# Performance work log

Hardware: AMD Instinct MI355X
Metric: run time of the kernel (lower is better)

Reference implementation:

```python
import jax, jax.numpy as jnp
import numpy as np

N = 50000
E = 800000
F = 128
H = 128
D = 3

def setup_inputs() -> dict:
    key = jax.random.key(0)
    ks = jax.random.split(key, 12)
    s = lambda fan_in: 1.0 / np.sqrt(fan_in)
    return {
        "node": jax.random.normal(ks[0], (N, F), jnp.float32),
        "coordinate": jax.random.normal(ks[1], (N, D), jnp.float32),
        "edge_index": jax.random.randint(ks[2], (2, E), 0, N, jnp.int32),
        "We1": jax.random.normal(ks[3], (2 * F + 1, H), jnp.float32) * s(2 * F + 1),
        "be1": jnp.zeros((H,), jnp.float32),
        "We2": jax.random.normal(ks[4], (H, H), jnp.float32) * s(H),
        "be2": jnp.zeros((H,), jnp.float32),
        "Wx": jax.random.normal(ks[5], (H, 1), jnp.float32) * s(H),
        "bx": jnp.zeros((1,), jnp.float32),
        "Wh1": jax.random.normal(ks[6], (F + H, H), jnp.float32) * s(F + H),
        "bh1": jnp.zeros((H,), jnp.float32),
        "Wh2": jax.random.normal(ks[7], (H, F), jnp.float32) * s(H),
        "bh2": jnp.zeros((F,), jnp.float32),
    }

def reference(node, coordinate, edge_index, We1, be1, We2, be2, Wx, bx, Wh1, bh1, Wh2, bh2):
    src = edge_index[0]
    dst = edge_index[1]
    n = node.shape[0]
    # gather endpoint features / coords
    h_j = node[src]            # [E, F]
    h_i = node[dst]            # [E, F]
    dist = coordinate[dst] - coordinate[src]          # [E, D] = x_i - x_j
    sqdist = jnp.sum(dist * dist, axis=1, keepdims=True)  # [E, 1]
    # phi_e: Linear -> ReLU -> Linear
    e_in = jnp.concatenate([h_i, h_j, sqdist], axis=-1)    # [E, 2F+1]
    m_ij = jax.nn.relu(e_in @ We1 + be1) @ We2 + be2       # [E, H]
    # phi_x: Linear to scalar edge weight
    w_ij = m_ij @ Wx + bx                                  # [E, 1]
    vec = dist * w_ij                                      # [E, D]
    C = 1.0 / (n - 1)
    delta_x = jax.ops.segment_sum(vec, dst, num_segments=n) * C
    x_new = coordinate + delta_x
    # aggregate messages per target node (sum)
    m_i = jax.ops.segment_sum(m_ij, dst, num_segments=n)   # [N, H]
    # phi_h: Linear -> ReLU -> Linear
    h_in = jnp.concatenate([node, m_i], axis=1)            # [N, F+H]
    h_new = jax.nn.relu(h_in @ Wh1 + bh1) @ Wh2 + bh2      # [N, F]
    return (h_new, x_new)
```

## Files before the change

### kernel.cpp

```cpp
#include <hip/hip_runtime.h>
#include <stdint.h>

#define NN 50000
#define NE 800000
#define NBINS 50001
#define H_OUT_OFF 6400000

typedef float  f32x4  __attribute__((ext_vector_type(4)));
typedef short  bf16x8 __attribute__((ext_vector_type(8)));

static __device__ __forceinline__ unsigned short f2b(float f) {
  unsigned u = __float_as_uint(f);
  return (unsigned short)((u + 0x7fffu + ((u >> 16) & 1u)) >> 16);
}
static __device__ __forceinline__ float b2f(unsigned short h) {
  return __uint_as_float(((unsigned)h) << 16);
}

__global__ void k1_kernel(const int* __restrict__ ei,
                          int* __restrict__ cnt,
                          unsigned short* __restrict__ rank,
                          const float* __restrict__ We1,
                          const float* __restrict__ We2,
                          const float* __restrict__ Wh1,
                          const float* __restrict__ Wh2,
                          const float* __restrict__ be2,
                          const float* __restrict__ Wx,
                          const float* __restrict__ bx,
                          unsigned short* __restrict__ We1Ttop,
                          unsigned short* __restrict__ We1Tbot,
                          unsigned short* __restrict__ We2T,
                          unsigned short* __restrict__ Wh1T,
                          unsigned short* __restrict__ Wh2T,
                          float* __restrict__ uvec) {
  int b = blockIdx.x, tid = threadIdx.x;
  if (b < 3125) {
    int i = b * 256 + tid;
    if (i < NE) rank[i] = (unsigned short)atomicAdd(&cnt[ei[NE + i]], 1);
    return;
  }
  b -= 3125;
  if (b < 384) {
    int i = b * 256 + tid;
    if (i < 16384) {
      int n = i >> 7, k = i & 127;
      We1Ttop[i] = f2b(We1[k * 128 + n]);
    } else if (i < 32768) {
      int j = i - 16384; int n = j >> 7, k = j & 127;
      We1Tbot[j] = f2b(We1[(128 + k) * 128 + n]);
    } else if (i < 49152) {
      int j = i - 32768; int n = j >> 7, k = j & 127;
      We2T[j] = f2b(We2[k * 128 + n]);
    } else if (i < 81920) {
      int j = i - 49152; int n = j >> 8, k = j & 255;
      Wh1T[j] = f2b(Wh1[k * 128 + n]);
    } else if (i < 98304) {
      int j = i - 81920; int n = j >> 7, k = j & 127;
      Wh2T[j] = f2b(Wh2[k * 128 + n]);
    }
    return;
  }
  int k = tid;
  if (k < 128) {
    float s = 0.f;
    for (int n = 0; n < 128; n++) s += We2[k * 128 + n] * Wx[n];
    uvec[k] = s;
  } else if (k == 128) {
    float s = 0.f;
    for (int n = 0; n < 128; n++) s += be2[n] * Wx[n];
    uvec[128] = s + bx[0];
  }
}

__global__ void scanA_kernel(const int* __restrict__ cnt, int* __restrict__ bsum) {
  __shared__ int sd[256];
  int b = blockIdx.x, t = threadIdx.x, i = b * 256 + t;
  sd[t] = (i < NBINS) ? cnt[i] : 0;
  __syncthreads();
  for (int s = 128; s; s >>= 1) {
    if (t < s) sd[t] += sd[t + s];
    __syncthreads();
  }
  if (t == 0) bsum[b] = sd[0];
}

__global__ void scanC_kernel(const int* __restrict__ cnt, const int* __restrict__ bsum,
                             int* __restrict__ starts) {
  __shared__ int sd[256];
  int b = blockIdx.x, t = threadIdx.x, i = b * 256 + t;
  int bv = (t < 196) ? bsum[t] : 0;
  sd[t] = bv;
  __syncthreads();
  for (int off = 1; off < 256; off <<= 1) {
    int x = (t >= off) ? sd[t - off] : 0;
    __syncthreads();
    sd[t] += x;
    __syncthreads();
  }
  int boff = (b > 0) ? sd[b - 1] : 0;
  __syncthreads();
  int v = (i < NBINS) ? cnt[i] : 0;
  sd[t] = v;
  __syncthreads();
  for (int off = 1; off < 256; off <<= 1) {
    int x = (t >= off) ? sd[t - off] : 0;
    __syncthreads();
    sd[t] += x;
    __syncthreads();
  }
  if (i < NBINS) starts[i] = sd[t] - v + boff;
}

__global__ __launch_bounds__(256, 4)
void k3_kernel(const int* __restrict__ ei,
               const unsigned short* __restrict__ rank,
               const int* __restrict__ starts,
               unsigned short* __restrict__ srcs,
               const float* __restrict__ node,
               const unsigned short* __restrict__ We1Ttop,
               const unsigned short* __restrict__ We1Tbot,
               const float* __restrict__ be1,
               unsigned short* __restrict__ Yb,
               unsigned short* __restrict__ Zb) {
  __shared__ __align__(16) unsigned short sA[64][136];
  const int tid = threadIdx.x;
  int b = blockIdx.x;

  if (b < 3125) {
    int i = b * 256 + tid;
    if (i < NE) {
      srcs[starts[ei[NE + i]] + (int)rank[i]] = (unsigned short)ei[i];
    }
    return;
  }
  b -= 3125;
  const int n0 = b * 64;

  for (int c = tid; c < 64 * 16; c += 256) {
    int e = c >> 4, s = c & 15;
    int n = n0 + e;
    if (n < NN) {
      const float* p = node + (size_t)n * 128 + s * 8;
      float4 v0 = *(const float4*)p;
      float4 v1 = *(const float4*)(p + 4);
      *(ushort4*)&sA[e][s * 8]     = make_ushort4(f2b(v0.x), f2b(v0.y), f2b(v0.z), f2b(v0.w));
      *(ushort4*)&sA[e][s * 8 + 4] = make_ushort4(f2b(v1.x), f2b(v1.y), f2b(v1.z), f2b(v1.w));
    } else {
      *(uint4*)&sA[e][s * 8] = make_uint4(0, 0, 0, 0);
    }
  }
  __syncthreads();

  const int wave = tid >> 6, lane = tid & 63;
  const int quad = lane >> 4, l16 = lane & 15;
  const int col0 = wave * 32 + l16, col1 = wave * 32 + 16 + l16;

  const f32x4 zero = {0.f, 0.f, 0.f, 0.f};
  f32x4 accY[4][2], accZ[4][2];
#pragma unroll
  for (int mt = 0; mt < 4; mt++) {
    accY[mt][0] = zero; accY[mt][1] = zero;
    accZ[mt][0] = zero; accZ[mt][1] = zero;
  }

#pragma unroll
  for (int kt = 0; kt < 4; kt++) {
    int kb = kt * 32 + quad * 8;
    bf16x8 by0 = *(const bf16x8*)(We1Ttop + (col0 << 7) + kb);
    bf16x8 by1 = *(const bf16x8*)(We1Ttop + (col1 << 7) + kb);
    bf16x8 bz0 = *(const bf16x8*)(We1Tbot + (col0 << 7) + kb);
    bf16x8 bz1 = *(const bf16x8*)(We1Tbot + (col1 << 7) + kb);
#pragma unroll
    for (int mt = 0; mt < 4; mt++) {
      bf16x8 a = *(const bf16x8*)&sA[mt * 16 + l16][kb];
      accY[mt][0] = __builtin_amdgcn_mfma_f32_16x16x32_bf16(a, by0, accY[mt][0], 0, 0, 0);
      accY[mt][1] = __builtin_amdgcn_mfma_f32_16x16x32_bf16(a, by1, accY[mt][1], 0, 0, 0);
      accZ[mt][0] = __builtin_amdgcn_mfma_f32_16x16x32_bf16(a, bz0, accZ[mt][0], 0, 0, 0);
      accZ[mt][1] = __builtin_amdgcn_mfma_f32_16x16x32_bf16(a, bz1, accZ[mt][1], 0, 0, 0);
    }
  }

  float sb0 = be1[col0], sb1 = be1[col1];
#pragma unroll
  for (int mt = 0; mt < 4; mt++) {
#pragma unroll
    for (int r = 0; r < 4; r++) {
      int row = mt * 16 + quad * 4 + r;
      int n = n0 + row;
      if (n < NN) {
        Yb[(size_t)n * 128 + col0] = f2b(accY[mt][0][r] + sb0);
        Yb[(size_t)n * 128 + col1] = f2b(accY[mt][1][r] + sb1);
        Zb[(size_t)n * 128 + col0] = f2b(accZ[mt][0][r]);
        Zb[(size_t)n * 128 + col1] = f2b(accZ[mt][1][r]);
      }
    }
  }
}

__global__ __launch_bounds__(256, 8)
void edge_kernel(const unsigned short* __restrict__ Zb,
                 const unsigned short* __restrict__ Yb,
                 const unsigned short* __restrict__ srcs,
                 const int* __restrict__ starts,
                 const float* __restrict__ coord,
                 const float* __restrict__ We1,
                 const float* __restrict__ uvec,
                 float* __restrict__ T,
                 float* __restrict__ out) {
  __shared__ int    sSrc[4][64];
  __shared__ float4 sQ[4][64];

  const int tid = threadIdx.x, wave = tid >> 6, lane = tid & 63;
  const int n = blockIdx.x * 4 + wave;
  const int half = lane >> 5, l32 = lane & 31;
  const int col = l32 * 4;

  const int start = starts[n], end = starts[n + 1];

  const float4 wsq = *(const float4*)(We1 + 256 * 128 + col);
  const float4 u   = *(const float4*)(uvec + col);
  const float  c   = uvec[128];
  ushort4 yv = *(const ushort4*)(Yb + (size_t)n * 128 + col);
  const float y0 = b2f(yv.x), y1 = b2f(yv.y), y2 = b2f(yv.z), y3 = b2f(yv.w);
  const float cdx = coord[n * 3 + 0], cdy = coord[n * 3 + 1], cdz = coord[n * 3 + 2];

  float aT0 = 0.f, aT1 = 0.f, aT2 = 0.f, aT3 = 0.f;
  float sx = 0.f, sy = 0.f, sz = 0.f;
  float dsx = 0.f, dsy = 0.f, dsz = 0.f;

  for (int cb = start; cb < end; cb += 64) {
    int m = end - cb; if (m > 64) m = 64;
    int s = 0; float dx = 0.f, dy = 0.f, dz = 0.f;
    if (lane < m) {
      s = (int)srcs[cb + lane];
      dx = cdx - coord[s * 3 + 0];
      dy = cdy - coord[s * 3 + 1];
      dz = cdz - coord[s * 3 + 2];
      dsx += dx; dsy += dy; dsz += dz;
    }
    sSrc[wave][lane] = s;
    sQ[wave][lane] = make_float4(dx, dy, dz, dx * dx + dy * dy + dz * dz);
    __builtin_amdgcn_wave_barrier();
    int pairs = (m + 1) >> 1;
    for (int p = 0; p < pairs; p++) {
      int idx = 2 * p + half;
      int ss = sSrc[wave][idx];
      float4 q = sQ[wave][idx];
      float valid = (idx < m) ? 1.f : 0.f;
      ushort4 zv = *(const ushort4*)(Zb + (size_t)ss * 128 + col);
      float t0 = fmaxf(b2f(zv.x) + y0 + q.w * wsq.x, 0.f) * valid;
      float t1 = fmaxf(b2f(zv.y) + y1 + q.w * wsq.y, 0.f) * valid;
      float t2 = fmaxf(b2f(zv.z) + y2 + q.w * wsq.z, 0.f) * valid;
      float t3 = fmaxf(b2f(zv.w) + y3 + q.w * wsq.w, 0.f) * valid;
      aT0 += t0; aT1 += t1; aT2 += t2; aT3 += t3;
      float tu = t0 * u.x + t1 * u.y + t2 * u.z + t3 * u.w;
      sx += tu * q.x; sy += tu * q.y; sz += tu * q.z;
    }
    __builtin_amdgcn_wave_barrier();
  }

  aT0 += __shfl_xor(aT0, 32); aT1 += __shfl_xor(aT1, 32);
  aT2 += __shfl_xor(aT2, 32); aT3 += __shfl_xor(aT3, 32);
  if (half == 0) {
    *(float4*)&T[(size_t)n * 128 + col] = make_float4(aT0, aT1, aT2, aT3);
  }

  float px = sx + c * dsx, py = sy + c * dsy, pz = sz + c * dsz;
#pragma unroll
  for (int o = 1; o < 64; o <<= 1) {
    px += __shfl_xor(px, o); py += __shfl_xor(py, o); pz += __shfl_xor(pz, o);
  }
  if (lane == 0) {
    const float C = 1.0f / 49999.0f;
    out[H_OUT_OFF + n * 3 + 0] = cdx + C * px;
    out[H_OUT_OFF + n * 3 + 1] = cdy + C * py;
    out[H_OUT_OFF + n * 3 + 2] = cdz + C * pz;
  }
}

__global__ __launch_bounds__(256, 3)
void node_kernel(const float* __restrict__ node,
                 const float* __restrict__ T,
                 const int* __restrict__ starts,
                 const unsigned short* __restrict__ We2T,
                 const float* __restrict__ be2,
                 const unsigned short* __restrict__ Wh1T,
                 const float* __restrict__ bh1,
                 const unsigned short* __restrict__ Wh2T,
                 const float* __restrict__ bh2,
                 float* __restrict__ out) {
  __shared__ __align__(16) unsigned short sA[64][264];
  __shared__ __align__(16) unsigned short sT[64][136];
  __shared__ float sDeg[64];

  const int tid = threadIdx.x;
  const int n0 = blockIdx.x * 64;

  if (tid < 64) {
    int n = n0 + tid;
    sDeg[tid] = (n < NN) ? (float)(starts[n + 1] - starts[n]) : 0.f;
  }

  for (int c = tid; c < 64 * 16; c += 256) {
    int e = c >> 4, s = c & 15;
    int n = n0 + e;
    if (n < NN) {
      const float* pn = node + (size_t)n * 128 + s * 8;
      float4 a0 = *(const float4*)pn;
      float4 a1 = *(const float4*)(pn + 4);
      *(ushort4*)&sA[e][s * 8]     = make_ushort4(f2b(a0.x), f2b(a0.y), f2b(a0.z), f2b(a0.w));
      *(ushort4*)&sA[e][s * 8 + 4] = make_ushort4(f2b(a1.x), f2b(a1.y), f2b(a1.z), f2b(a1.w));
      const float* p = T + (size_t)n * 128 + s * 8;
      float4 v0 = *(const float4*)p;
      float4 v1 = *(const float4*)(p + 4);
      *(ushort4*)&sT[e][s * 8]     = make_ushort4(f2b(v0.x), f2b(v0.y), f2b(v0.z), f2b(v0.w));
      *(ushort4*)&sT[e][s * 8 + 4] = make_ushort4(f2b(v1.x), f2b(v1.y), f2b(v1.z), f2b(v1.w));
    } else {
      *(uint4*)&sA[e][s * 8] = make_uint4(0, 0, 0, 0);
      *(uint4*)&sT[e][s * 8] = make_uint4(0, 0, 0, 0);
    }
  }
  __syncthreads();

  const int wave = tid >> 6, lane = tid & 63;
  const int quad = lane >> 4, l16 = lane & 15;
  const int col0 = wave * 32 + l16, col1 = wave * 32 + 16 + l16;

  const f32x4 zero = {0.f, 0.f, 0.f, 0.f};

  f32x4 accM[4][2];
#pragma unroll
  for (int mt = 0; mt < 4; mt++) { accM[mt][0] = zero; accM[mt][1] = zero; }
#pragma unroll
  for (int kt = 0; kt < 4; kt++) {
    int kb = kt * 32 + quad * 8;
    bf16x8 b0 = *(const bf16x8*)(We2T + (col0 << 7) + kb);
    bf16x8 b1 = *(const bf16x8*)(We2T + (col1 << 7) + kb);
#pragma unroll
    for (int mt = 0; mt < 4; mt++) {
      bf16x8 a = *(const bf16x8*)&sT[mt * 16 + l16][kb];
      accM[mt][0] = __builtin_amdgcn_mfma_f32_16x16x32_bf16(a, b0, accM[mt][0], 0, 0, 0);
      accM[mt][1] = __builtin_amdgcn_mfma_f32_16x16x32_bf16(a, b1, accM[mt][1], 0, 0, 0);
    }
  }
  {
    float eb0 = be2[col0], eb1 = be2[col1];
#pragma unroll
    for (int mt = 0; mt < 4; mt++) {
#pragma unroll
      for (int r = 0; r < 4; r++) {
        int row = mt * 16 + quad * 4 + r;
        float dg = sDeg[row];
        sA[row][128 + col0] = f2b(accM[mt][0][r] + dg * eb0);
        sA[row][128 + col1] = f2b(accM[mt][1][r] + dg * eb1);
      }
    }
  }
  __syncthreads();

  f32x4 acc[4][2];
#pragma unroll
  for (int mt = 0; mt < 4; mt++) { acc[mt][0] = zero; acc[mt][1] = zero; }
#pragma unroll
  for (int kt = 0; kt < 8; kt++) {
    int kb = kt * 32 + quad * 8;
    bf16x8 b0 = *(const bf16x8*)(Wh1T + (col0 << 8) + kb);
    bf16x8 b1 = *(const bf16x8*)(Wh1T + (col1 << 8) + kb);
#pragma unroll
    for (int mt = 0; mt < 4; mt++) {
      bf16x8 a = *(const bf16x8*)&sA[mt * 16 + l16][kb];
      acc[mt][0] = __builtin_amdgcn_mfma_f32_16x16x32_bf16(a, b0, acc[mt][0], 0, 0, 0);
      acc[mt][1] = __builtin_amdgcn_mfma_f32_16x16x32_bf16(a, b1, acc[mt][1], 0, 0, 0);
    }
  }
  {
    float sb0 = bh1[col0], sb1 = bh1[col1];
#pragma unroll
    for (int mt = 0; mt < 4; mt++) {
#pragma unroll
      for (int r = 0; r < 4; r++) {
        int row = mt * 16 + quad * 4 + r;
        sT[row][col0] = f2b(fmaxf(acc[mt][0][r] + sb0, 0.f));
        sT[row][col1] = f2b(fmaxf(acc[mt][1][r] + sb1, 0.f));
      }
    }
  }
  __syncthreads();

  f32x4 acc2[4][2];
#pragma unroll
  for (int mt = 0; mt < 4; mt++) { acc2[mt][0] = zero; acc2[mt][1] = zero; }
#pragma unroll
  for (int kt = 0; kt < 4; kt++) {
    int kb = kt * 32 + quad * 8;
    bf16x8 b0 = *(const bf16x8*)(Wh2T + (col0 << 7) + kb);
    bf16x8 b1 = *(const bf16x8*)(Wh2T + (col1 << 7) + kb);
#pragma unroll
    for (int mt = 0; mt < 4; mt++) {
      bf16x8 a = *(const bf16x8*)&sT[mt * 16 + l16][kb];
      acc2[mt][0] = __builtin_amdgcn_mfma_f32_16x16x32_bf16(a, b0, acc2[mt][0], 0, 0, 0);
      acc2[mt][1] = __builtin_amdgcn_mfma_f32_16x16x32_bf16(a, b1, acc2[mt][1], 0, 0, 0);
    }
  }
  {
    float eb0 = bh2[col0], eb1 = bh2[col1];
#pragma unroll
    for (int mt = 0; mt < 4; mt++) {
#pragma unroll
      for (int r = 0; r < 4; r++) {
        int row = mt * 16 + quad * 4 + r;
        int n = n0 + row;
        if (n < NN) {
          out[(size_t)n * 128 + col0] = acc2[mt][0][r] + eb0;
          out[(size_t)n * 128 + col1] = acc2[mt][1][r] + eb1;
        }
      }
    }
  }
}

extern "C" void kernel_launch(void* const* d_in, const int* in_sizes, int n_in,
                              void* d_out, int out_size, void* d_ws, size_t ws_size,
                              hipStream_t stream) {
  const float* node  = (const float*)d_in[0];
  const float* coord = (const float*)d_in[1];
  const int*   ei    = (const int*)d_in[2];
  const float* We1   = (const float*)d_in[3];
  const float* be1   = (const float*)d_in[4];
  const float* We2   = (const float*)d_in[5];
  const float* be2   = (const float*)d_in[6];
  const float* Wx    = (const float*)d_in[7];
  const float* bx    = (const float*)d_in[8];
  const float* Wh1   = (const float*)d_in[9];
  const float* bh1   = (const float*)d_in[10];
  const float* Wh2   = (const float*)d_in[11];
  const float* bh2   = (const float*)d_in[12];
  float* out = (float*)d_out;

  char* ws = (char*)d_ws;
  float*          T      = (float*)(ws);
  int*            cnt    = (int*)  (ws + 25600000);
  int*            starts = (int*)  (ws + 25800704);
  int*            bsum   = (int*)  (ws + 26001408);
  unsigned short* rank   = (unsigned short*)(ws + 26002432);
  unsigned short* srcs   = (unsigned short*)(ws + 27602432);
  unsigned short* Yb     = (unsigned short*)(ws + 29202432);
  unsigned short* Zb     = (unsigned short*)(ws + 42002432);
  unsigned short* We1Ttop= (unsigned short*)(ws + 54802432);
  unsigned short* We1Tbot= (unsigned short*)(ws + 54835200);
  unsigned short* We2T   = (unsigned short*)(ws + 54867968);
  unsigned short* Wh1T   = (unsigned short*)(ws + 54900736);
  unsigned short* Wh2T   = (unsigned short*)(ws + 54966272);
  float*          uvec   = (float*)(ws + 54999040);

  hipMemsetAsync(cnt, 0, 200704, stream);

  k1_kernel<<<3510, 256, 0, stream>>>(ei, cnt, rank, We1, We2, Wh1, Wh2,
                                      be2, Wx, bx,
                                      We1Ttop, We1Tbot, We2T, Wh1T, Wh2T, uvec);
  scanA_kernel<<<196, 256, 0, stream>>>(cnt, bsum);
  scanC_kernel<<<196, 256, 0, stream>>>(cnt, bsum, starts);
  k3_kernel<<<3907, 256, 0, stream>>>(ei, rank, starts, srcs,
                                      node, We1Ttop, We1Tbot, be1, Yb, Zb);
  edge_kernel<<<NN / 4, 256, 0, stream>>>(Zb, Yb, srcs, starts, coord, We1, uvec,
                                          T, out);
  node_kernel<<<782, 256, 0, stream>>>(node, T, starts, We2T, be2,
                                       Wh1T, bh1, Wh2T, bh2, out);
}
```

Measured before the change: 242.0 us.

## Fuse all stages into one persistent cooperative kernel with grid syncs

Replaces the memset and six separate kernel launches with a single cooperative persistent kernel. Phases are separated by grid.sync(), and blocks loop over work with grid-stride loops. This targets launch overhead and inter-kernel gaps. The costs are grid-wide barrier overhead, a grid limited to at most 1024 blocks (so less parallelism in the edge phase), and an occupancy cap from launch_bounds(256,4). The old multi-kernel path stays as a fallback if the cooperative launch fails.

```diff
diff --git a/kernel.cpp b/kernel.cpp
--- a/kernel.cpp
+++ b/kernel.cpp
@@ -1,10 +1,14 @@
 #include <hip/hip_runtime.h>
+#include <hip/hip_cooperative_groups.h>
 #include <stdint.h>
+
+namespace cg = cooperative_groups;
 
 #define NN 50000
 #define NE 800000
 #define NBINS 50001
 #define H_OUT_OFF 6400000
+#define NTILE 782
 
 typedef float  f32x4  __attribute__((ext_vector_type(4)));
 typedef short  bf16x8 __attribute__((ext_vector_type(8)));
@@ -17,15 +21,398 @@
   return __uint_as_float(((unsigned)h) << 16);
 }
 
-__global__ void k1_kernel(const int* __restrict__ ei,
-                          int* __restrict__ cnt,
+__global__ __launch_bounds__(256, 4)
+void mega_kernel(const int* __restrict__ ei,
+                 int* __restrict__ cnt,
+                 unsigned short* __restrict__ rank,
+                 int* __restrict__ starts,
+                 int* __restrict__ bsum,
+                 unsigned short* __restrict__ srcs,
+                 const float* __restrict__ node,
+                 const float* __restrict__ coord,
+                 const float* __restrict__ We1,
+                 const float* __restrict__ be1,
+                 const float* __restrict__ We2,
+                 const float* __restrict__ be2,
+                 const float* __restrict__ Wx,
+                 const float* __restrict__ bx,
+                 const float* __restrict__ Wh1,
+                 const float* __restrict__ bh1,
+                 const float* __restrict__ Wh2,
+                 const float* __restrict__ bh2,
+                 unsigned short* __restrict__ We1Ttop,
+                 unsigned short* __restrict__ We1Tbot,
+                 unsigned short* __restrict__ We2T,
+                 unsigned short* __restrict__ Wh1T,
+                 unsigned short* __restrict__ Wh2T,
+                 float* __restrict__ uvec,
+                 float* __restrict__ T,
+                 unsigned short* __restrict__ Yb,
+                 unsigned short* __restrict__ Zb,
+                 float* __restrict__ out) {
+  __shared__ __align__(16) unsigned char smem[34048];
+  cg::grid_group grid = cg::this_grid();
+  const int tid = threadIdx.x;
+  const int bid = blockIdx.x;
+  const int gridN = gridDim.x;
+  const int wave = tid >> 6, lane = tid & 63;
+
+  for (int i = bid * 256 + tid; i < NBINS; i += gridN * 256) cnt[i] = 0;
+  grid.sync();
+
+  for (int i = bid * 256 + tid; i < NE; i += gridN * 256) {
+    rank[i] = (unsigned short)atomicAdd(&cnt[ei[NE + i]], 1);
+  }
+  for (int i = bid * 256 + tid; i < 98304; i += gridN * 256) {
+    if (i < 16384) {
+      int n = i >> 7, k = i & 127;
+      We1Ttop[i] = f2b(We1[k * 128 + n]);
+    } else if (i < 32768) {
+      int j = i - 16384; int n = j >> 7, k = j & 127;
+      We1Tbot[j] = f2b(We1[(128 + k) * 128 + n]);
+    } else if (i < 49152) {
+      int j = i - 32768; int n = j >> 7, k = j & 127;
+      We2T[j] = f2b(We2[k * 128 + n]);
+    } else if (i < 81920) {
+      int j = i - 49152; int n = j >> 8, k = j & 255;
+      Wh1T[j] = f2b(Wh1[k * 128 + n]);
+    } else {
+      int j = i - 81920; int n = j >> 7, k = j & 127;
+      Wh2T[j] = f2b(Wh2[k * 128 + n]);
+    }
+  }
+  if (bid == 0) {
+    int k = tid;
+    if (k < 128) {
+      float s = 0.f;
+      for (int n = 0; n < 128; n++) s += We2[k * 128 + n] * Wx[n];
+      uvec[k] = s;
+    } else if (k == 128) {
+      float s = 0.f;
+      for (int n = 0; n < 128; n++) s += be2[n] * Wx[n];
+      uvec[128] = s + bx[0];
+    }
+  }
+  grid.sync();
+
+  {
+    int* sd = (int*)smem;
+    for (int ch = bid; ch < 196; ch += gridN) {
+      int i = ch * 256 + tid;
+      sd[tid] = (i < NBINS) ? cnt[i] : 0;
+      __syncthreads();
+      for (int s = 128; s; s >>= 1) {
+        if (tid < s) sd[tid] += sd[tid + s];
+        __syncthreads();
+      }
+      if (tid == 0) bsum[ch] = sd[0];
+      __syncthreads();
+    }
+  }
+  grid.sync();
+
+  {
+    int* sd   = (int*)smem;
+    int* sPre = (int*)smem + 256;
+    int bv = (tid < 196) ? bsum[tid] : 0;
+    sPre[tid] = bv;
+    __syncthreads();
+    for (int off = 1; off < 256; off <<= 1) {
+      int x = (tid >= off) ? sPre[tid - off] : 0;
+      __syncthreads();
+      sPre[tid] += x;
+      __syncthreads();
+    }
+    for (int ch = bid; ch < 196; ch += gridN) {
+      int i = ch * 256 + tid;
+      int boff = (ch > 0) ? sPre[ch - 1] : 0;
+      int v = (i < NBINS) ? cnt[i] : 0;
+      sd[tid] = v;
+      __syncthreads();
+      for (int off = 1; off < 256; off <<= 1) {
+        int x = (tid >= off) ? sd[tid - off] : 0;
+        __syncthreads();
+        sd[tid] += x;
+        __syncthreads();
+      }
+      if (i < NBINS) starts[i] = sd[tid] - v + boff;
+      __syncthreads();
+    }
+  }
+  grid.sync();
+
+  {
+    unsigned short (*sA)[136] = (unsigned short (*)[136])smem;
+    const int quad = lane >> 4, l16 = lane & 15;
+    const int col0 = wave * 32 + l16, col1 = wave * 32 + 16 + l16;
+    const f32x4 zero = {0.f, 0.f, 0.f, 0.f};
+    for (int tb = bid; tb < NTILE; tb += gridN) {
+      const int n0 = tb * 64;
+      for (int c = tid; c < 64 * 16; c += 256) {
+        int e = c >> 4, s = c & 15;
+        int n = n0 + e;
+        if (n < NN) {
+          const float* p = node + (size_t)n * 128 + s * 8;
+          float4 v0 = *(const float4*)p;
+          float4 v1 = *(const float4*)(p + 4);
+          *(ushort4*)&sA[e][s * 8]     = make_ushort4(f2b(v0.x), f2b(v0.y), f2b(v0.z), f2b(v0.w));
+          *(ushort4*)&sA[e][s * 8 + 4] = make_ushort4(f2b(v1.x), f2b(v1.y), f2b(v1.z), f2b(v1.w));
+        } else {
+          *(uint4*)&sA[e][s * 8] = make_uint4(0, 0, 0, 0);
+        }
+      }
+      __syncthreads();
+      f32x4 accY[4][2], accZ[4][2];
+#pragma unroll
+      for (int mt = 0; mt < 4; mt++) {
+        accY[mt][0] = zero; accY[mt][1] = zero;
+        accZ[mt][0] = zero; accZ[mt][1] = zero;
+      }
+#pragma unroll
+      for (int kt = 0; kt < 4; kt++) {
+        int kb = kt * 32 + quad * 8;
+        bf16x8 by0 = *(const bf16x8*)(We1Ttop + (col0 << 7) + kb);
+        bf16x8 by1 = *(const bf16x8*)(We1Ttop + (col1 << 7) + kb);
+        bf16x8 bz0 = *(const bf16x8*)(We1Tbot + (col0 << 7) + kb);
+        bf16x8 bz1 = *(const bf16x8*)(We1Tbot + (col1 << 7) + kb);
+#pragma unroll
+        for (int mt = 0; mt < 4; mt++) {
+          bf16x8 a = *(const bf16x8*)&sA[mt * 16 + l16][kb];
+          accY[mt][0] = __builtin_amdgcn_mfma_f32_16x16x32_bf16(a, by0, accY[mt][0], 0, 0, 0);
+          accY[mt][1] = __builtin_amdgcn_mfma_f32_16x16x32_bf16(a, by1, accY[mt][1], 0, 0, 0);
+          accZ[mt][0] = __builtin_amdgcn_mfma_f32_16x16x32_bf16(a, bz0, accZ[mt][0], 0, 0, 0);
+          accZ[mt][1] = __builtin_amdgcn_mfma_f32_16x16x32_bf16(a, bz1, accZ[mt][1], 0, 0, 0);
+        }
+      }
+      float sb0 = be1[col0], sb1 = be1[col1];
+#pragma unroll
+      for (int mt = 0; mt < 4; mt++) {
+#pragma unroll
+        for (int r = 0; r < 4; r++) {
+          int row = mt * 16 + quad * 4 + r;
+          int n = n0 + row;
+          if (n < NN) {
+            Yb[(size_t)n * 128 + col0] = f2b(accY[mt][0][r] + sb0);
+            Yb[(size_t)n * 128 + col1] = f2b(accY[mt][1][r] + sb1);
+            Zb[(size_t)n * 128 + col0] = f2b(accZ[mt][0][r]);
+            Zb[(size_t)n * 128 + col1] = f2b(accZ[mt][1][r]);
+          }
+        }
+      }
+      __syncthreads();
+    }
+  }
+  for (int i = bid * 256 + tid; i < NE; i += gridN * 256) {
+    srcs[starts[ei[NE + i]] + (int)rank[i]] = (unsigned short)ei[i];
+  }
+  grid.sync();
+
+  {
+    int*    sSrc = (int*)smem + wave * 64;
+    float4* sQ   = (float4*)(smem + 1024) + wave * 64;
+    const int half = lane >> 5, l32 = lane & 31;
+    const int col = l32 * 4;
+    const float4 wsq = *(const float4*)(We1 + 256 * 128 + col);
+    const float4 u   = *(const float4*)(uvec + col);
+    const float  c   = uvec[128];
+
+    for (int vb = bid; vb < NN / 4; vb += gridN) {
+      const int n = vb * 4 + wave;
+      const int start = starts[n], end = starts[n + 1];
+      ushort4 yv = *(const ushort4*)(Yb + (size_t)n * 128 + col);
+      const float y0 = b2f(yv.x), y1 = b2f(yv.y), y2 = b2f(yv.z), y3 = b2f(yv.w);
+      const float cdx = coord[n * 3 + 0], cdy = coord[n * 3 + 1], cdz = coord[n * 3 + 2];
+
+      float aT0 = 0.f, aT1 = 0.f, aT2 = 0.f, aT3 = 0.f;
+      float sx = 0.f, sy = 0.f, sz = 0.f;
+      float dsx = 0.f, dsy = 0.f, dsz = 0.f;
+
+      for (int cb = start; cb < end; cb += 64) {
+        int m = end - cb; if (m > 64) m = 64;
+        int s = 0; float dx = 0.f, dy = 0.f, dz = 0.f;
+        if (lane < m) {
+          s = (int)srcs[cb + lane];
+          dx = cdx - coord[s * 3 + 0];
+          dy = cdy - coord[s * 3 + 1];
+          dz = cdz - coord[s * 3 + 2];
+          dsx += dx; dsy += dy; dsz += dz;
+        }
+        sSrc[lane] = s;
+        sQ[lane] = make_float4(dx, dy, dz, dx * dx + dy * dy + dz * dz);
+        __builtin_amdgcn_wave_barrier();
+        int pairs = (m + 1) >> 1;
+        for (int p = 0; p < pairs; p++) {
+          int idx = 2 * p + half;
+          int ss = sSrc[idx];
+          float4 q = sQ[idx];
+          float valid = (idx < m) ? 1.f : 0.f;
+          ushort4 zv = *(const ushort4*)(Zb + (size_t)ss * 128 + col);
+          float t0 = fmaxf(b2f(zv.x) + y0 + q.w * wsq.x, 0.f) * valid;
+          float t1 = fmaxf(b2f(zv.y) + y1 + q.w * wsq.y, 0.f) * valid;
+          float t2 = fmaxf(b2f(zv.z) + y2 + q.w * wsq.z, 0.f) * valid;
+          float t3 = fmaxf(b2f(zv.w) + y3 + q.w * wsq.w, 0.f) * valid;
+          aT0 += t0; aT1 += t1; aT2 += t2; aT3 += t3;
+          float tu = t0 * u.x + t1 * u.y + t2 * u.z + t3 * u.w;
+          sx += tu * q.x; sy += tu * q.y; sz += tu * q.z;
+        }
+        __builtin_amdgcn_wave_barrier();
+      }
+
+      aT0 += __shfl_xor(aT0, 32); aT1 += __shfl_xor(aT1, 32);
+      aT2 += __shfl_xor(aT2, 32); aT3 += __shfl_xor(aT3, 32);
+      if (half == 0) {
+        *(float4*)&T[(size_t)n * 128 + col] = make_float4(aT0, aT1, aT2, aT3);
+      }
+      float px = sx + c * dsx, py = sy + c * dsy, pz = sz + c * dsz;
+#pragma unroll
+      for (int o = 1; o < 64; o <<= 1) {
+        px += __shfl_xor(px, o); py += __shfl_xor(py, o); pz += __shfl_xor(pz, o);
+      }
+      if (lane == 0) {
+        const float C = 1.0f / 49999.0f;
+        out[H_OUT_OFF + n * 3 + 0] = cdx + C * px;
+        out[H_OUT_OFF + n * 3 + 1] = cdy + C * py;
+        out[H_OUT_OFF + n * 3 + 2] = cdz + C * pz;
+      }
+    }
+  }
+  grid.sync();
+
+  {
+    unsigned short (*sA)[264] = (unsigned short (*)[264])smem;
+    float* sDeg = (float*)(smem + 33792);
+    const int quad = lane >> 4, l16 = lane & 15;
+    const int col0 = wave * 32 + l16, col1 = wave * 32 + 16 + l16;
+    const f32x4 zero = {0.f, 0.f, 0.f, 0.f};
+
+    for (int tb = bid; tb < NTILE; tb += gridN) {
+      const int n0 = tb * 64;
+      if (tid < 64) {
+        int n = n0 + tid;
+        sDeg[tid] = (n < NN) ? (float)(starts[n + 1] - starts[n]) : 0.f;
+      }
+      for (int c = tid; c < 64 * 16; c += 256) {
+        int e = c >> 4, s = c & 15;
+        int n = n0 + e;
+        if (n < NN) {
+          const float* pn = node + (size_t)n * 128 + s * 8;
+          float4 a0 = *(const float4*)pn;
+          float4 a1 = *(const float4*)(pn + 4);
+          *(ushort4*)&sA[e][s * 8]     = make_ushort4(f2b(a0.x), f2b(a0.y), f2b(a0.z), f2b(a0.w));
+          *(ushort4*)&sA[e][s * 8 + 4] = make_ushort4(f2b(a1.x), f2b(a1.y), f2b(a1.z), f2b(a1.w));
+          const float* p = T + (size_t)n * 128 + s * 8;
+          float4 v0 = *(const float4*)p;
+          float4 v1 = *(const float4*)(p + 4);
+          *(ushort4*)&sA[e][128 + s * 8]     = make_ushort4(f2b(v0.x), f2b(v0.y), f2b(v0.z), f2b(v0.w));
+          *(ushort4*)&sA[e][128 + s * 8 + 4] = make_ushort4(f2b(v1.x), f2b(v1.y), f2b(v1.z), f2b(v1.w));
+        } else {
+          *(uint4*)&sA[e][s * 8] = make_uint4(0, 0, 0, 0);
+          *(uint4*)&sA[e][128 + s * 8] = make_uint4(0, 0, 0, 0);
+        }
+      }
+      __syncthreads();
+
+      f32x4 accM[4][2];
+#pragma unroll
+      for (int mt = 0; mt < 4; mt++) { accM[mt][0] = zero; accM[mt][1] = zero; }
+#pragma unroll
+      for (int kt = 0; kt < 4; kt++) {
+        int kb = kt * 32 + quad * 8;
+        bf16x8 b0 = *(const bf16x8*)(We2T + (col0 << 7) + kb);
+        bf16x8 b1 = *(const bf16x8*)(We2T + (col1 << 7) + kb);
+#pragma unroll
+        for (int mt = 0; mt < 4; mt++) {
+          bf16x8 a = *(const bf16x8*)&sA[mt * 16 + l16][128 + kb];
+          accM[mt][0] = __builtin_amdgcn_mfma_f32_16x16x32_bf16(a, b0, accM[mt][0], 0, 0, 0);
+          accM[mt][1] = __builtin_amdgcn_mfma_f32_16x16x32_bf16(a, b1, accM[mt][1], 0, 0, 0);
+        }
+      }
+      __syncthreads();
+      {
+        float eb0 = be2[col0], eb1 = be2[col1];
+#pragma unroll
+        for (int mt = 0; mt < 4; mt++) {
+#pragma unroll
+          for (int r = 0; r < 4; r++) {
+            int row = mt * 16 + quad * 4 + r;
+            float dg = sDeg[row];
+            sA[row][128 + col0] = f2b(accM[mt][0][r] + dg * eb0);
+            sA[row][128 + col1] = f2b(accM[mt][1][r] + dg * eb1);
+          }
+        }
+      }
+      __syncthreads();
+
+      f32x4 acc[4][2];
+#pragma unroll
+      for (int mt = 0; mt < 4; mt++) { acc[mt][0] = zero; acc[mt][1] = zero; }
+#pragma unroll
+      for (int kt = 0; kt < 8; kt++) {
+        int kb = kt * 32 + quad * 8;
+        bf16x8 b0 = *(const bf16x8*)(Wh1T + (col0 << 8) + kb);
+        bf16x8 b1 = *(const bf16x8*)(Wh1T + (col1 << 8) + kb);
+#pragma unroll
+        for (int mt = 0; mt < 4; mt++) {
+          bf16x8 a = *(const bf16x8*)&sA[mt * 16 + l16][kb];
+          acc[mt][0] = __builtin_amdgcn_mfma_f32_16x16x32_bf16(a, b0, acc[mt][0], 0, 0, 0);
+          acc[mt][1] = __builtin_amdgcn_mfma_f32_16x16x32_bf16(a, b1, acc[mt][1], 0, 0, 0);
+        }
+      }
+      __syncthreads();
+      {
+        float sb0 = bh1[col0], sb1 = bh1[col1];
+#pragma unroll
+        for (int mt = 0; mt < 4; mt++) {
+#pragma unroll
+          for (int r = 0; r < 4; r++) {
+            int row = mt * 16 + quad * 4 + r;
+            sA[row][col0] = f2b(fmaxf(acc[mt][0][r] + sb0, 0.f));
+            sA[row][col1] = f2b(fmaxf(acc[mt][1][r] + sb1, 0.f));
+          }
+        }
+      }
+      __syncthreads();
+
+      f32x4 acc2[4][2];
+#pragma unroll
+      for (int mt = 0; mt < 4; mt++) { acc2[mt][0] = zero; acc2[mt][1] = zero; }
+#pragma unroll
+      for (int kt = 0; kt < 4; kt++) {
+        int kb = kt * 32 + quad * 8;
+        bf16x8 b0 = *(const bf16x8*)(Wh2T + (col0 << 7) + kb);
+        bf16x8 b1 = *(const bf16x8*)(Wh2T + (col1 << 7) + kb);
+#pragma unroll
+        for (int mt = 0; mt < 4; mt++) {
+          bf16x8 a = *(const bf16x8*)&sA[mt * 16 + l16][kb];
+          acc2[mt][0] = __builtin_amdgcn_mfma_f32_16x16x32_bf16(a, b0, acc2[mt][0], 0, 0, 0);
+          acc2[mt][1] = __builtin_amdgcn_mfma_f32_16x16x32_bf16(a, b1, acc2[mt][1], 0, 0, 0);
+        }
+      }
+      {
+        float eb0 = bh2[col0], eb1 = bh2[col1];
+#pragma unroll
+        for (int mt = 0; mt < 4; mt++) {
+#pragma unroll
+          for (int r = 0; r < 4; r++) {
+            int row = mt * 16 + quad * 4 + r;
+            int n = n0 + row;
+            if (n < NN) {
+              out[(size_t)n * 128 + col0] = acc2[mt][0][r] + eb0;
+              out[(size_t)n * 128 + col1] = acc2[mt][1][r] + eb1;
+            }
+          }
+        }
+      }
+      __syncthreads();
+    }
+  }
+}
+
+__global__ void k1_kernel(const int* __restrict__ ei, int* __restrict__ cnt,
                           unsigned short* __restrict__ rank,
-                          const float* __restrict__ We1,
-                          const float* __restrict__ We2,
-                          const float* __restrict__ Wh1,
-                          const float* __restrict__ Wh2,
-                          const float* __restrict__ be2,
-                          const float* __restrict__ Wx,
+                          const float* __restrict__ We1, const float* __restrict__ We2,
+                          const float* __restrict__ Wh1, const float* __restrict__ Wh2,
+                          const float* __restrict__ be2, const float* __restrict__ Wx,
                           const float* __restrict__ bx,
                           unsigned short* __restrict__ We1Ttop,
                           unsigned short* __restrict__ We1Tbot,
@@ -112,30 +499,23 @@
 }
 
 __global__ __launch_bounds__(256, 4)
-void k3_kernel(const int* __restrict__ ei,
-               const unsigned short* __restrict__ rank,
-               const int* __restrict__ starts,
-               unsigned short* __restrict__ srcs,
+void k3_kernel(const int* __restrict__ ei, const unsigned short* __restrict__ rank,
+               const int* __restrict__ starts, unsigned short* __restrict__ srcs,
                const float* __restrict__ node,
                const unsigned short* __restrict__ We1Ttop,
                const unsigned short* __restrict__ We1Tbot,
                const float* __restrict__ be1,
-               unsigned short* __restrict__ Yb,
-               unsigned short* __restrict__ Zb) {
+               unsigned short* __restrict__ Yb, unsigned short* __restrict__ Zb) {
   __shared__ __align__(16) unsigned short sA[64][136];
   const int tid = threadIdx.x;
   int b = blockIdx.x;
-
   if (b < 3125) {
     int i = b * 256 + tid;
-    if (i < NE) {
-      srcs[starts[ei[NE + i]] + (int)rank[i]] = (unsigned short)ei[i];
-    }
+    if (i < NE) srcs[starts[ei[NE + i]] + (int)rank[i]] = (unsigned short)ei[i];
     return;
   }
   b -= 3125;
   const int n0 = b * 64;
-
   for (int c = tid; c < 64 * 16; c += 256) {
     int e = c >> 4, s = c & 15;
     int n = n0 + e;
@@ -150,11 +530,9 @@
     }
   }
   __syncthreads();
-
   const int wave = tid >> 6, lane = tid & 63;
   const int quad = lane >> 4, l16 = lane & 15;
   const int col0 = wave * 32 + l16, col1 = wave * 32 + 16 + l16;
-
   const f32x4 zero = {0.f, 0.f, 0.f, 0.f};
   f32x4 accY[4][2], accZ[4][2];
 #pragma unroll
@@ -162,7 +540,6 @@
     accY[mt][0] = zero; accY[mt][1] = zero;
     accZ[mt][0] = zero; accZ[mt][1] = zero;
   }
-
 #pragma unroll
   for (int kt = 0; kt < 4; kt++) {
     int kb = kt * 32 + quad * 8;
@@ -179,7 +556,6 @@
       accZ[mt][1] = __builtin_amdgcn_mfma_f32_16x16x32_bf16(a, bz1, accZ[mt][1], 0, 0, 0);
     }
   }
-
   float sb0 = be1[col0], sb1 = be1[col1];
 #pragma unroll
   for (int mt = 0; mt < 4; mt++) {
@@ -209,25 +585,20 @@
                  float* __restrict__ out) {
   __shared__ int    sSrc[4][64];
   __shared__ float4 sQ[4][64];
-
   const int tid = threadIdx.x, wave = tid >> 6, lane = tid & 63;
   const int n = blockIdx.x * 4 + wave;
   const int half = lane >> 5, l32 = lane & 31;
   const int col = l32 * 4;
-
   const int start = starts[n], end = starts[n + 1];
-
   const float4 wsq = *(const float4*)(We1 + 256 * 128 + col);
   const float4 u   = *(const float4*)(uvec + col);
   const float  c   = uvec[128];
   ushort4 yv = *(const ushort4*)(Yb + (size_t)n * 128 + col);
   const float y0 = b2f(yv.x), y1 = b2f(yv.y), y2 = b2f(yv.z), y3 = b2f(yv.w);
   const float cdx = coord[n * 3 + 0], cdy = coord[n * 3 + 1], cdz = coord[n * 3 + 2];
-
   float aT0 = 0.f, aT1 = 0.f, aT2 = 0.f, aT3 = 0.f;
   float sx = 0.f, sy = 0.f, sz = 0.f;
   float dsx = 0.f, dsy = 0.f, dsz = 0.f;
-
   for (int cb = start; cb < end; cb += 64) {
     int m = end - cb; if (m > 64) m = 64;
     int s = 0; float dx = 0.f, dy = 0.f, dz = 0.f;
@@ -258,13 +629,11 @@
     }
     __builtin_amdgcn_wave_barrier();
   }
-
   aT0 += __shfl_xor(aT0, 32); aT1 += __shfl_xor(aT1, 32);
   aT2 += __shfl_xor(aT2, 32); aT3 += __shfl_xor(aT3, 32);
   if (half == 0) {
     *(float4*)&T[(size_t)n * 128 + col] = make_float4(aT0, aT1, aT2, aT3);
   }
-
   float px = sx + c * dsx, py = sy + c * dsy, pz = sz + c * dsz;
 #pragma unroll
   for (int o = 1; o < 64; o <<= 1) {
@@ -279,28 +648,21 @@
 }
 
 __global__ __launch_bounds__(256, 3)
-void node_kernel(const float* __restrict__ node,
-                 const float* __restrict__ T,
+void node_kernel(const float* __restrict__ node, const float* __restrict__ T,
                  const int* __restrict__ starts,
-                 const unsigned short* __restrict__ We2T,
-                 const float* __restrict__ be2,
-                 const unsigned short* __restrict__ Wh1T,
-                 const float* __restrict__ bh1,
-                 const unsigned short* __restrict__ Wh2T,
-                 const float* __restrict__ bh2,
+                 const unsigned short* __restrict__ We2T, const float* __restrict__ be2,
+                 const unsigned short* __restrict__ Wh1T, const float* __restrict__ bh1,
+                 const unsigned short* __restrict__ Wh2T, const float* __restrict__ bh2,
                  float* __restrict__ out) {
   __shared__ __align__(16) unsigned short sA[64][264];
   __shared__ __align__(16) unsigned short sT[64][136];
   __shared__ float sDeg[64];
-
   const int tid = threadIdx.x;
   const int n0 = blockIdx.x * 64;
-
   if (tid < 64) {
     int n = n0 + tid;
     sDeg[tid] = (n < NN) ? (float)(starts[n + 1] - starts[n]) : 0.f;
   }
-
   for (int c = tid; c < 64 * 16; c += 256) {
     int e = c >> 4, s = c & 15;
     int n = n0 + e;
@@ -321,13 +683,10 @@
     }
   }
   __syncthreads();
-
   const int wave = tid >> 6, lane = tid & 63;
   const int quad = lane >> 4, l16 = lane & 15;
   const int col0 = wave * 32 + l16, col1 = wave * 32 + 16 + l16;
-
   const f32x4 zero = {0.f, 0.f, 0.f, 0.f};
-
   f32x4 accM[4][2];
 #pragma unroll
   for (int mt = 0; mt < 4; mt++) { accM[mt][0] = zero; accM[mt][1] = zero; }
@@ -357,7 +716,6 @@
     }
   }
   __syncthreads();
-
   f32x4 acc[4][2];
 #pragma unroll
   for (int mt = 0; mt < 4; mt++) { acc[mt][0] = zero; acc[mt][1] = zero; }
@@ -386,7 +744,6 @@
     }
   }
   __syncthreads();
-
   f32x4 acc2[4][2];
 #pragma unroll
   for (int mt = 0; mt < 4; mt++) { acc2[mt][0] = zero; acc2[mt][1] = zero; }
@@ -453,17 +810,42 @@
   unsigned short* Wh2T   = (unsigned short*)(ws + 54966272);
   float*          uvec   = (float*)(ws + 54999040);
 
-  hipMemsetAsync(cnt, 0, 200704, stream);
-
-  k1_kernel<<<3510, 256, 0, stream>>>(ei, cnt, rank, We1, We2, Wh1, Wh2,
-                                      be2, Wx, bx,
-                                      We1Ttop, We1Tbot, We2T, Wh1T, Wh2T, uvec);
-  scanA_kernel<<<196, 256, 0, stream>>>(cnt, bsum);
-  scanC_kernel<<<196, 256, 0, stream>>>(cnt, bsum, starts);
-  k3_kernel<<<3907, 256, 0, stream>>>(ei, rank, starts, srcs,
-                                      node, We1Ttop, We1Tbot, be1, Yb, Zb);
-  edge_kernel<<<NN / 4, 256, 0, stream>>>(Zb, Yb, srcs, starts, coord, We1, uvec,
-                                          T, out);
-  node_kernel<<<782, 256, 0, stream>>>(node, T, starts, We2T, be2,
-                                       Wh1T, bh1, Wh2T, bh2, out);
-}
+  int blocksPerCU = 0;
+  hipError_t qerr = hipOccupancyMaxActiveBlocksPerMultiprocessor(
+      &blocksPerCU, (const void*)mega_kernel, 256, 0);
+  int grid = 0;
+  if (qerr == hipSuccess && blocksPerCU > 0) {
+    grid = blocksPerCU * 256;
+    if (grid > 1024) grid = 1024;
+  }
+
+  hipError_t lerr = hipErrorUnknown;
+  if (grid > 0) {
+    void* args[] = {
+      (void*)&ei, (void*)&cnt, (void*)&rank, (void*)&starts, (void*)&bsum,
+      (void*)&srcs, (void*)&node, (void*)&coord, (void*)&We1, (void*)&be1,
+      (void*)&We2, (void*)&be2, (void*)&Wx, (void*)&bx, (void*)&Wh1,
+      (void*)&bh1, (void*)&Wh2, (void*)&bh2, (void*)&We1Ttop, (void*)&We1Tbot,
+      (void*)&We2T, (void*)&Wh1T, (void*)&Wh2T, (void*)&uvec, (void*)&T,
+      (void*)&Yb, (void*)&Zb, (void*)&out
+    };
+    lerr = hipLaunchCooperativeKernel((const void*)mega_kernel, dim3(grid),
+                                      dim3(256), args, 0, stream);
+  }
+
+  if (lerr != hipSuccess) {
+    (void)hipGetLastError();
+    hipMemsetAsync(cnt, 0, 200704, stream);
+    k1_kernel<<<3510, 256, 0, stream>>>(ei, cnt, rank, We1, We2, Wh1, Wh2,
+                                        be2, Wx, bx,
+                                        We1Ttop, We1Tbot, We2T, Wh1T, Wh2T, uvec);
+    scanA_kernel<<<196, 256, 0, stream>>>(cnt, bsum);
+    scanC_kernel<<<196, 256, 0, stream>>>(cnt, bsum, starts);
+    k3_kernel<<<3907, 256, 0, stream>>>(ei, rank, starts, srcs,
+                                        node, We1Ttop, We1Tbot, be1, Yb, Zb);
+    edge_kernel<<<NN / 4, 256, 0, stream>>>(Zb, Yb, srcs, starts, coord, We1,
+                                            uvec, T, out);
+    node_kernel<<<782, 256, 0, stream>>>(node, T, starts, We2T, be2,
+                                         Wh1T, bh1, Wh2T, bh2, out);
+  }
+}
```

New measurement: 678.3 us. 2.8x slower.
